# Kernel tuning notes

Measured on AMD Instinct MI355X. Metric: run time of the kernel, lower is better.

Reference implementation:

```python
import jax, jax.numpy as jnp
import numpy as np

N = 50000
E = 800000
DESC = 256
IN_CH = DESC + 64  # 320
HEADS = 4
HC = 64  # hidden_channels // heads
HID = HEADS * HC  # 256


def _lin(k, fan_in, fan_out):
    kw, kb = jax.random.split(k)
    s = 1.0 / np.sqrt(fan_in)
    W = jax.random.uniform(kw, (fan_in, fan_out), minval=-s, maxval=s, dtype=jnp.float32)
    b = jax.random.uniform(kb, (fan_out,), minval=-s, maxval=s, dtype=jnp.float32)
    return W, b


def setup_inputs() -> dict:
    key = jax.random.key(0)
    ks = jax.random.split(key, 16)
    x = jax.random.normal(ks[0], (N, DESC), dtype=jnp.float32)
    kpts = jax.random.uniform(ks[1], (N, 2), dtype=jnp.float32) * jnp.array([1216.0, 352.0])
    pts_3d = jax.random.uniform(ks[2], (N, 3), dtype=jnp.float32) * 10.0
    edge_index = jax.random.randint(ks[3], (2, E), 0, N, dtype=jnp.int64)

    W1, b1 = _lin(ks[4], 3, 32)
    W2, b2 = _lin(ks[5], 32, 64)
    Wres, bres = _lin(ks[6], IN_CH, HID)
    Wl, bl = _lin(ks[7], IN_CH, HID)
    Wr, br = _lin(ks[8], IN_CH, HID)
    We, _ = _lin(ks[9], 3, HID)
    att = jax.random.normal(ks[10], (HEADS, HC), dtype=jnp.float32) * 0.1
    conv_bias = jnp.zeros((HID,), dtype=jnp.float32)
    gamma = jnp.ones((HID,), dtype=jnp.float32)
    beta = jnp.zeros((HID,), dtype=jnp.float32)
    Wp, bp = _lin(ks[11], HID, 256)
    return dict(x=x, kpts=kpts, pts_3d=pts_3d, edge_index=edge_index,
                W1=W1, b1=b1, W2=W2, b2=b2, Wres=Wres, bres=bres,
                Wl=Wl, bl=bl, Wr=Wr, br=br, We=We, att=att, conv_bias=conv_bias,
                gamma=gamma, beta=beta, Wp=Wp, bp=bp)


def reference(x, kpts, pts_3d, edge_index, W1, b1, W2, b2, Wres, bres,
              Wl, bl, Wr, br, We, att, conv_bias, gamma, beta, Wp, bp):
    n = x.shape[0]
    norm_uv = kpts / jnp.array([1216.0, 352.0], dtype=kpts.dtype)
    depth = pts_3d[:, 2:3]
    pos_input = jnp.concatenate([norm_uv, depth], axis=-1)  # [N,3]
    pos_feat = jax.nn.silu(pos_input @ W1 + b1) @ W2 + b2   # [N,64]
    node_x = jnp.concatenate([x, pos_feat], axis=-1)        # [N,320]

    src, dst = edge_index[0], edge_index[1]
    rel_uv = norm_uv[dst] - norm_uv[src]                    # [E,2]
    dist = jnp.linalg.norm(rel_uv, axis=-1, keepdims=True)  # [E,1]
    edge_attr = jnp.concatenate([rel_uv, dist], axis=-1)    # [E,3]

    identity = node_x @ Wres + bres                         # [N,256]

    # GATv2Conv (share_weights=False, concat=True, neg_slope=0.2, no self-loops)
    x_l = (node_x @ Wl + bl).reshape(n, HEADS, HC)
    x_r = (node_x @ Wr + br).reshape(n, HEADS, HC)
    e_feat = (edge_attr @ We).reshape(-1, HEADS, HC)        # [E,H,C]

    m = x_l[src] + x_r[dst] + e_feat                        # [E,H,C]
    m = jnp.where(m >= 0, m, 0.2 * m)                       # LeakyReLU(0.2)
    logits = jnp.einsum('ehc,hc->eh', m, att)               # [E,H]

    # segment softmax over incoming edges of each dst node
    lmax = jax.ops.segment_max(logits, dst, num_segments=n)  # [N,H]
    ex = jnp.exp(logits - lmax[dst])
    denom = jax.ops.segment_sum(ex, dst, num_segments=n)     # [N,H]
    alpha = ex / (denom[dst] + 1e-16)                        # [E,H]

    msg = x_l[src] * alpha[:, :, None]                       # [E,H,C]
    out = jax.ops.segment_sum(msg, dst, num_segments=n).reshape(n, HID) + conv_bias

    # LayerNorm
    mu = out.mean(-1, keepdims=True)
    var = out.var(-1, keepdims=True)
    out = (out - mu) / jnp.sqrt(var + 1e-5) * gamma + beta

    out = jax.nn.silu(out)
    out = out + identity
    out = out @ Wp + bp
    return out, alpha
```

## Files before the change

### kernel.cpp

```cpp
#include <hip/hip_runtime.h>
#include <math.h>

#define NN 50000
#define NPAD 50048
#define EE 800000
#define HIDC 256
#define INCH 320

typedef __attribute__((ext_vector_type(8))) short bf16x8;
typedef __attribute__((ext_vector_type(4))) float f32x4;
typedef __attribute__((ext_vector_type(2))) float f32x2;

static __device__ __forceinline__ float4 ld4(const float* p){ return *(const float4*)p; }

static __device__ __forceinline__ unsigned short f2b(float f){
  union { float f; unsigned u; } v; v.f = f;
  unsigned r = v.u + 0x7fffu + ((v.u >> 16) & 1u);
  return (unsigned short)(r >> 16);
}
static __device__ __forceinline__ float b2f(unsigned short u){
  union { unsigned u; float f; } v; v.u = ((unsigned)u) << 16; return v.f;
}
static __device__ __forceinline__ float rlane_f(float v, int l){
  return __uint_as_float(__builtin_amdgcn_readlane(__float_as_uint(v), l));
}
static __device__ __forceinline__ int rlane_i(int v, int l){
  return __builtin_amdgcn_readlane(v, l);
}
static __device__ __forceinline__ f32x2 unpk(unsigned u){
  f32x2 r;
  r.x = __uint_as_float(u << 16);
  r.y = __uint_as_float(u & 0xffff0000u);
  return r;
}
static __device__ __forceinline__ f32x2 fma2(f32x2 a, f32x2 b, f32x2 c){
  return __builtin_elementwise_fma(a, b, c);
}
static __device__ __forceinline__ f32x2 max2(f32x2 a, f32x2 b){
  return __builtin_elementwise_max(a, b);
}
static __device__ __forceinline__ f32x2 set2(float v){ f32x2 r; r.x = v; r.y = v; return r; }

typedef const __attribute__((address_space(1))) unsigned int* gas_u32;
typedef __attribute__((address_space(3))) unsigned int* las_u32;
static __device__ __forceinline__ void gload_lds16(const void* g, void* l){
  __builtin_amdgcn_global_load_lds((gas_u32)g, (las_u32)l, 16, 0, 0);
}

__global__ void cvt_x_kernel(const float* __restrict__ x, unsigned short* __restrict__ nodex)
{
  int t = blockIdx.x*blockDim.x + threadIdx.x;
  int row = t >> 6;
  if (row >= NN) return;
  int c4 = (t & 63) * 4;
  float4 v = ld4(x + (size_t)row*256 + c4);
  ushort4 o;
  o.x = f2b(v.x); o.y = f2b(v.y); o.z = f2b(v.z); o.w = f2b(v.w);
  *(ushort4*)(nodex + (size_t)row*320 + c4) = o;
}

__global__ void node_mlp_kernel(const float* __restrict__ kpts,
                                const float* __restrict__ pts3d,
                                const float* __restrict__ W1, const float* __restrict__ b1,
                                const float* __restrict__ W2, const float* __restrict__ b2,
                                unsigned short* __restrict__ nodex)
{
  int i = blockIdx.x*blockDim.x + threadIdx.x;
  if (i >= NN) return;
  float u = kpts[2*i]   * (1.0f/1216.0f);
  float v = kpts[2*i+1] * (1.0f/352.0f);
  float d = pts3d[3*i+2];
  float h[32];
#pragma unroll
  for (int j=0;j<32;++j){
    float t = u*W1[j] + v*W1[32+j] + d*W1[64+j] + b1[j];
    h[j] = t / (1.0f + __expf(-t));
  }
  for (int o=0;o<64;o+=4){
    float s0=b2[o], s1=b2[o+1], s2=b2[o+2], s3=b2[o+3];
#pragma unroll
    for (int j=0;j<32;++j){
      float hj = h[j];
      const float* w = W2 + j*64 + o;
      s0 += hj*w[0]; s1 += hj*w[1]; s2 += hj*w[2]; s3 += hj*w[3];
    }
    ushort4 r; r.x=f2b(s0); r.y=f2b(s1); r.z=f2b(s2); r.w=f2b(s3);
    *(ushort4*)(nodex + (size_t)i*320 + 256 + o) = r;
  }
}

__global__ void cvt_w_kernel(const float* __restrict__ Wres, const float* __restrict__ Wl,
                             const float* __restrict__ Wr,   const float* __restrict__ Wp,
                             const float* __restrict__ bres, const float* __restrict__ bl,
                             const float* __restrict__ br,
                             unsigned short* __restrict__ wt, float* __restrict__ biascat)
{
  int t = blockIdx.x*blockDim.x + threadIdx.x;
  if (t < 245760) {
    int which = t / 81920;
    int rem = t % 81920;
    int n = rem / 320, k = rem % 320;
    const float* W = (which == 0) ? Wres : (which == 1) ? Wl : Wr;
    wt[(size_t)which*81920 + rem] = f2b(W[(size_t)k*256 + n]);
  } else if (t < 311296) {
    int r = t - 245760;
    int n = r / 256, k = r % 256;
    wt[245760 + r] = f2b(Wp[(size_t)k*256 + n]);
  } else {
    int r = t - 311296;
    const float* src = (r < 256) ? bres : (r < 512) ? bl : br;
    biascat[r] = src[r & 255];
  }
}

#define GK 32
__global__ __launch_bounds__(256) void mfma_gemm_kernel(
    const unsigned short* __restrict__ A,
    const unsigned short* __restrict__ BT,
    const float* __restrict__ bias,
    float* __restrict__ Cf,
    unsigned short* __restrict__ Cx1,
    unsigned short* __restrict__ Cx2,
    int M, int K)
{
  __shared__ unsigned short Als[128*GK];
  __shared__ unsigned short Bls[128*GK];
  int tid = threadIdx.x;
  int lane = tid & 63, wave = tid >> 6;
  int wm = (wave >> 1) * 64, wn = (wave & 1) * 64;
  int row0 = blockIdx.x * 128, col0 = blockIdx.y * 128;

  f32x4 acc[4][4];
#pragma unroll
  for (int i=0;i<4;++i)
#pragma unroll
    for (int j=0;j<4;++j){ acc[i][j].x=0.f; acc[i][j].y=0.f; acc[i][j].z=0.f; acc[i][j].w=0.f; }

  int fm = lane & 15;
  int fk = (lane >> 4) * 8;

  for (int k0 = 0; k0 < K; k0 += GK) {
#pragma unroll
    for (int it = 0; it < 2; ++it) {
      int seg = it*256 + tid;
      int r = seg >> 2, kb = (seg & 3) * 8;
      gload_lds16(A  + (size_t)(row0 + r)*K + k0 + kb, Als + (it*256 + wave*64)*8);
      gload_lds16(BT + (size_t)(col0 + r)*K + k0 + kb, Bls + (it*256 + wave*64)*8);
    }
    __syncthreads();

    bf16x8 af[4], bfr[4];
#pragma unroll
    for (int mi=0; mi<4; ++mi)
      af[mi] = *(const bf16x8*)&Als[(wm + mi*16 + fm)*GK + fk];
#pragma unroll
    for (int ni=0; ni<4; ++ni)
      bfr[ni] = *(const bf16x8*)&Bls[(wn + ni*16 + fm)*GK + fk];
#pragma unroll
    for (int mi=0; mi<4; ++mi)
#pragma unroll
      for (int ni=0; ni<4; ++ni)
        acc[mi][ni] = __builtin_amdgcn_mfma_f32_16x16x32_bf16(af[mi], bfr[ni], acc[mi][ni], 0, 0, 0);
    __syncthreads();
  }

  int seg = col0 >> 8;
  int colbase = col0 - seg*256;
  int cn = lane & 15, cr = (lane >> 4) * 4;
#pragma unroll
  for (int ni=0; ni<4; ++ni){
    int gcol = col0 + wn + ni*16 + cn;
    int col  = colbase + wn + ni*16 + cn;
    float bb = bias[gcol];
#pragma unroll
    for (int mi=0; mi<4; ++mi){
#pragma unroll
      for (int r=0; r<4; ++r){
        int row = row0 + wm + mi*16 + cr + r;
        if (row < M){
          float v = acc[mi][ni][r] + bb;
          if (seg == 0)      Cf [(size_t)row*256 + col] = v;
          else if (seg == 1) Cx1[(size_t)row*256 + col] = f2b(v);
          else               Cx2[(size_t)row*256 + col] = f2b(v);
        }
      }
    }
  }
}

__global__ void hist_kernel(const int* __restrict__ ei, int* __restrict__ deg){
  int e = blockIdx.x*blockDim.x + threadIdx.x;
  if (e < EE) atomicAdd(&deg[ei[EE + e]], 1);
}

__global__ __launch_bounds__(1024) void scan1_kernel(const int* __restrict__ deg,
                                                     int* __restrict__ incl, int* __restrict__ bsum){
  __shared__ int wsums[16];
  int t = threadIdx.x, lane = t & 63, w = t >> 6;
  int i = blockIdx.x*1024 + t;
  int v = (i < NN) ? deg[i] : 0;
  int sc = v;
#pragma unroll
  for (int off = 1; off < 64; off <<= 1) {
    int o = __shfl_up(sc, off, 64);
    if (lane >= off) sc += o;
  }
  if (lane == 63) wsums[w] = sc;
  __syncthreads();
  if (w == 0) {
    int ws = (lane < 16) ? wsums[lane] : 0;
#pragma unroll
    for (int off = 1; off < 16; off <<= 1) {
      int o = __shfl_up(ws, off, 64);
      if (lane >= off) ws += o;
    }
    if (lane < 16) wsums[lane] = ws;
  }
  __syncthreads();
  int woff = (w > 0) ? wsums[w-1] : 0;
  if (i < NN) incl[i] = sc + woff;
  if (t == 1023) bsum[blockIdx.x] = woff + sc;
}

__global__ void scan2_kernel(int* __restrict__ bsum, int nblk){
  int lane = threadIdx.x;
  int v = (lane < nblk) ? bsum[lane] : 0;
#pragma unroll
  for (int off = 1; off < 64; off <<= 1) {
    int o = __shfl_up(v, off, 64);
    if (lane >= off) v += o;
  }
  if (lane < nblk) bsum[lane] = v;
}

__global__ __launch_bounds__(1024) void scan3_kernel(const int* __restrict__ incl,
                                                     const int* __restrict__ deg,
                                                     const int* __restrict__ bsum,
                                                     int* __restrict__ rowptr, int* __restrict__ cursor,
                                                     int nblk){
  int i = blockIdx.x*1024 + threadIdx.x;
  if (i < NN) {
    int b = blockIdx.x;
    int prev = (b > 0) ? bsum[b-1] : 0;
    int ex = prev + incl[i] - deg[i];
    rowptr[i] = ex;
    cursor[i] = ex;
  }
  if (i == 0) rowptr[NN] = bsum[nblk-1];
}

__global__ void scatter_kernel(const int* __restrict__ ei, const float* __restrict__ kpts,
                               int* __restrict__ cursor,
                               float4* __restrict__ edata, int* __restrict__ eord){
  int e = blockIdx.x*blockDim.x + threadIdx.x;
  if (e >= EE) return;
  int s = ei[e];
  int d = ei[EE + e];
  int pos = atomicAdd(&cursor[d], 1);
  float su = kpts[2*s]   * (1.0f/1216.0f);
  float sv = kpts[2*s+1] * (1.0f/352.0f);
  float du = kpts[2*d]   * (1.0f/1216.0f);
  float dv = kpts[2*d+1] * (1.0f/352.0f);
  float ru = du - su, rv = dv - sv;
  float dist = sqrtf(ru*ru + rv*rv);
  float4 ed; ed.x = ru; ed.y = rv; ed.z = dist; ed.w = __int_as_float(s);
  edata[pos] = ed;
  eord[pos] = e;
}

#define LOAD8(Q, B0)                                               \
  if ((B0) < cnt) {                                                \
    _Pragma("unroll")                                              \
    for (int t = 0; t < 8; ++t) {                                  \
      int sj = rlane_i(s, ((B0) + t) & 63);                        \
      Q[t] = *(const uint2*)(xlp + ((size_t)sj << 8));             \
    }                                                              \
  }

#define PROC8(Q, B0)                                               \
  _Pragma("unroll")                                                \
  for (int t = 0; t < 8; ++t) {                                    \
    int j = (B0) + t;                                              \
    if (j < cnt) {                                                 \
      float ruj = rlane_f(ed.x, j);                                \
      float rvj = rlane_f(ed.y, j);                                \
      float dj  = rlane_f(ed.z, j);                                \
      f32x2 x01 = unpk(Q[t].x), x23 = unpk(Q[t].y);                \
      f32x2 t01 = fma2(set2(ruj), we0a, xr01);                     \
      t01 = fma2(set2(rvj), we1a, t01);                            \
      t01 = fma2(set2(dj),  we2a, t01);                            \
      t01 = t01 + x01;                                             \
      f32x2 t23 = fma2(set2(ruj), we0b, xr23);                     \
      t23 = fma2(set2(rvj), we1b, t23);                            \
      t23 = fma2(set2(dj),  we2b, t23);                            \
      t23 = t23 + x23;                                             \
      t01 = max2(t01, t01*0.2f);                                   \
      t23 = max2(t23, t23*0.2f);                                   \
      f32x2 pd = t01*atta;                                         \
      pd = fma2(t23, attb, pd);                                    \
      float p = pd.x + pd.y;                                       \
      p += __shfl_xor(p, 1, 64);                                   \
      p += __shfl_xor(p, 2, 64);                                   \
      p += __shfl_xor(p, 4, 64);                                   \
      p += __shfl_xor(p, 8, 64);                                   \
      float exv = __expf(p);                                       \
      denom += exv;                                                \
      int ej = rlane_i(e, j);                                      \
      if ((lane & 15) == 0) alpha_out[(size_t)ej*4 + head] = exv;  \
      f32x2 ex2 = set2(exv);                                       \
      agg01 = fma2(ex2, x01, agg01);                               \
      agg23 = fma2(ex2, x23, agg23);                               \
    }                                                              \
  }

__global__ __launch_bounds__(256) void node_attn_kernel(
    const float4* __restrict__ edata, const int* __restrict__ eord,
    const unsigned short* __restrict__ xl, const unsigned short* __restrict__ xr,
    const float* __restrict__ We, const float* __restrict__ att,
    const float* __restrict__ cbias, const float* __restrict__ gamma,
    const float* __restrict__ beta,
    const int* __restrict__ rowptr,
    const float* __restrict__ identity,
    float* __restrict__ alpha_out, float* __restrict__ denom_buf,
    unsigned short* __restrict__ hbuf)
{
  int wid  = threadIdx.x >> 6;
  int lane = threadIdx.x & 63;
  int v = blockIdx.x*4 + wid;
  if (v >= NN) return;
  int c0 = lane*4;
  int head = lane >> 4;

  f32x2 we0a, we0b, we1a, we1b, we2a, we2b, atta, attb;
  we0a.x = We[c0];       we0a.y = We[c0+1];       we0b.x = We[c0+2];       we0b.y = We[c0+3];
  we1a.x = We[256+c0];   we1a.y = We[256+c0+1];   we1b.x = We[256+c0+2];   we1b.y = We[256+c0+3];
  we2a.x = We[512+c0];   we2a.y = We[512+c0+1];   we2b.x = We[512+c0+2];   we2b.y = We[512+c0+3];
  atta.x = att[c0];      atta.y = att[c0+1];      attb.x = att[c0+2];      attb.y = att[c0+3];
  uint2 xrq = *(const uint2*)(xr + (size_t)v*256 + c0);
  f32x2 xr01 = unpk(xrq.x), xr23 = unpk(xrq.y);
  const unsigned short* xlp = xl + c0;

  int rs = rowptr[v], re = rowptr[v+1];
  int deg = re - rs;

  float denom = 0.f;
  f32x2 agg01 = set2(0.f), agg23 = set2(0.f);

  for (int base = 0; base < deg; base += 64) {
    int cnt = min(64, deg - base);
    float4 ed; ed.x = 0.f; ed.y = 0.f; ed.z = 0.f; ed.w = __int_as_float(0);
    int e = 0;
    if (lane < cnt) {
      ed = edata[rs + base + lane];
      e  = eord [rs + base + lane];
    }
    int s = __float_as_int(ed.w);

    uint2 qa[8], qb[8];
    LOAD8(qa, 0);
    for (int b0 = 0; b0 < cnt; b0 += 16) {
      LOAD8(qb, b0 + 8);
      PROC8(qa, b0);
      LOAD8(qa, b0 + 16);
      PROC8(qb, b0 + 8);
    }
  }

  float rdenom = 1.0f / (denom + 1e-16f);
  if ((lane & 15) == 0) denom_buf[(size_t)v*4 + head] = denom;

  float a0 = agg01.x*rdenom + cbias[c0];
  float a1 = agg01.y*rdenom + cbias[c0+1];
  float a2 = agg23.x*rdenom + cbias[c0+2];
  float a3 = agg23.y*rdenom + cbias[c0+3];

  float ps  = a0 + a1 + a2 + a3;
  float ps2 = a0*a0 + a1*a1 + a2*a2 + a3*a3;
#pragma unroll
  for (int off = 1; off < 64; off <<= 1) {
    ps  += __shfl_xor(ps,  off, 64);
    ps2 += __shfl_xor(ps2, off, 64);
  }
  float mu  = ps  * (1.0f/256.0f);
  float var = ps2 * (1.0f/256.0f) - mu*mu;
  float rstd = rsqrtf(var + 1e-5f);
  float4 g  = ld4(gamma + c0);
  float4 b  = ld4(beta  + c0);
  float4 idv = ld4(identity + (size_t)v*256 + c0);
  float y0 = (a0 - mu)*rstd*g.x + b.x;
  float y1 = (a1 - mu)*rstd*g.y + b.y;
  float y2 = (a2 - mu)*rstd*g.z + b.z;
  float y3 = (a3 - mu)*rstd*g.w + b.w;
  y0 = y0 / (1.0f + __expf(-y0)) + idv.x;
  y1 = y1 / (1.0f + __expf(-y1)) + idv.y;
  y2 = y2 / (1.0f + __expf(-y2)) + idv.z;
  y3 = y3 / (1.0f + __expf(-y3)) + idv.w;
  ushort4 hq; hq.x=f2b(y0); hq.y=f2b(y1); hq.z=f2b(y2); hq.w=f2b(y3);
  *(ushort4*)(hbuf + (size_t)v*256 + c0) = hq;
}

__global__ void alpha_fin_kernel(const int* __restrict__ ei, const float* __restrict__ denom_buf,
                                 float* __restrict__ alpha)
{
  int e = blockIdx.x*blockDim.x + threadIdx.x;
  if (e >= EE) return;
  int d = ei[EE + e];
  float4 dn = ld4(denom_buf + (size_t)d*4);
  float4 a = ld4(alpha + (size_t)e*4);
  a.x /= (dn.x + 1e-16f);
  a.y /= (dn.y + 1e-16f);
  a.z /= (dn.z + 1e-16f);
  a.w /= (dn.w + 1e-16f);
  *(float4*)(alpha + (size_t)e*4) = a;
}

extern "C" void kernel_launch(void* const* d_in, const int* in_sizes, int n_in,
                              void* d_out, int out_size, void* d_ws, size_t ws_size,
                              hipStream_t stream)
{
  const float* x      = (const float*)d_in[0];
  const float* kpts   = (const float*)d_in[1];
  const float* pts3d  = (const float*)d_in[2];
  const int*   ei     = (const int*)d_in[3];
  const float* W1     = (const float*)d_in[4];
  const float* b1     = (const float*)d_in[5];
  const float* W2     = (const float*)d_in[6];
  const float* b2     = (const float*)d_in[7];
  const float* Wres   = (const float*)d_in[8];
  const float* bres   = (const float*)d_in[9];
  const float* Wl     = (const float*)d_in[10];
  const float* bl     = (const float*)d_in[11];
  const float* Wr     = (const float*)d_in[12];
  const float* br     = (const float*)d_in[13];
  const float* We     = (const float*)d_in[14];
  const float* att    = (const float*)d_in[15];
  const float* cbias  = (const float*)d_in[16];
  const float* gamma  = (const float*)d_in[17];
  const float* beta   = (const float*)d_in[18];
  const float* Wp     = (const float*)d_in[19];
  const float* bp     = (const float*)d_in[20];

  float* out       = (float*)d_out;
  float* alpha_out = out + (size_t)NN*HIDC;

  float* wsf = (float*)d_ws;
  float*          identity = wsf;
  unsigned short* xl       = (unsigned short*)(wsf + 12800000);
  unsigned short* xr       = (unsigned short*)(wsf + 19206144);
  unsigned short* nodex    = (unsigned short*)(wsf + 25612288);
  unsigned short* hbuf     = (unsigned short*)(wsf + 25612288);
  unsigned short* wt       = (unsigned short*)(wsf + 33619968);
  float*          biascat  = wsf + 33775616;
  float*          denomb   = wsf + 33776384;
  float4*         edata    = (float4*)(wsf + 33976384);
  int*            eord     = (int*)(wsf + 37176384);
  int*            incl     = (int*)(wsf + 37176384);
  int*            deg      = (int*)(wsf + 37976384);
  int*            rowptr   = (int*)(wsf + 38026384);
  int*            cursor   = (int*)(wsf + 38076385);
  int*            bsum     = (int*)(wsf + 38126385);

  unsigned short* wtcat = wt;
  unsigned short* wtp   = wt + 245760;

  cvt_x_kernel<<<12500, 256, 0, stream>>>(x, nodex);
  node_mlp_kernel<<<(NN+255)/256, 256, 0, stream>>>(kpts, pts3d, W1, b1, W2, b2, nodex);
  cvt_w_kernel<<<1219, 256, 0, stream>>>(Wres, Wl, Wr, Wp, bres, bl, br, wt, biascat);

  dim3 g3(NPAD/128, 6);
  mfma_gemm_kernel<<<g3, 256, 0, stream>>>(nodex, wtcat, biascat, identity, xl, xr, NN, INCH);

  hipMemsetAsync(deg, 0, NN*sizeof(int), stream);
  hist_kernel<<<(EE+255)/256, 256, 0, stream>>>(ei, deg);
  int nblk = (NN + 1023) / 1024;
  scan1_kernel<<<nblk, 1024, 0, stream>>>(deg, incl, bsum);
  scan2_kernel<<<1, 64, 0, stream>>>(bsum, nblk);
  scan3_kernel<<<nblk, 1024, 0, stream>>>(incl, deg, bsum, rowptr, cursor, nblk);
  scatter_kernel<<<(EE+255)/256, 256, 0, stream>>>(ei, kpts, cursor, edata, eord);

  node_attn_kernel<<<(NN+3)/4, 256, 0, stream>>>(edata, eord, xl, xr, We, att,
                                                 cbias, gamma, beta,
                                                 rowptr, identity,
                                                 alpha_out, denomb, hbuf);
  alpha_fin_kernel<<<(EE+255)/256, 256, 0, stream>>>(ei, denomb, alpha_out);

  dim3 g1(NPAD/128, 2);
  mfma_gemm_kernel<<<g1, 256, 0, stream>>>(hbuf, wtp, bp, out, nullptr, nullptr, NN, HIDC);
}
```

Baseline: 552.1 us.

## Process two edges per wavefront using half-waves with wider per-lane loads

The node attention kernel now splits each 64-lane wavefront into two 32-lane halves. Each half processes a different incoming edge, and each lane covers 8 channels with 16-byte loads instead of 4 channels with 8-byte loads. Per-edge data is now loaded per lane with a software prefetch pipeline that runs two pairs ahead, replacing the batched readlane broadcasts. The goal is to halve the serial per-edge iteration count and the shuffle-reduction depth per edge. The cost is a cross-half reduction at the end, more registers, and idle lanes when the degree is odd.

```diff
diff --git a/kernel.cpp b/kernel.cpp
--- a/kernel.cpp
+++ b/kernel.cpp
@@ -20,12 +20,6 @@
 }
 static __device__ __forceinline__ float b2f(unsigned short u){
   union { unsigned u; float f; } v; v.u = ((unsigned)u) << 16; return v.f;
-}
-static __device__ __forceinline__ float rlane_f(float v, int l){
-  return __uint_as_float(__builtin_amdgcn_readlane(__float_as_uint(v), l));
-}
-static __device__ __forceinline__ int rlane_i(int v, int l){
-  return __builtin_amdgcn_readlane(v, l);
 }
 static __device__ __forceinline__ f32x2 unpk(unsigned u){
   f32x2 r;
@@ -268,49 +262,53 @@
   eord[pos] = e;
 }
 
-#define LOAD8(Q, B0)                                               \
-  if ((B0) < cnt) {                                                \
-    _Pragma("unroll")                                              \
-    for (int t = 0; t < 8; ++t) {                                  \
-      int sj = rlane_i(s, ((B0) + t) & 63);                        \
-      Q[t] = *(const uint2*)(xlp + ((size_t)sj << 8));             \
-    }                                                              \
-  }
-
-#define PROC8(Q, B0)                                               \
-  _Pragma("unroll")                                                \
-  for (int t = 0; t < 8; ++t) {                                    \
-    int j = (B0) + t;                                              \
-    if (j < cnt) {                                                 \
-      float ruj = rlane_f(ed.x, j);                                \
-      float rvj = rlane_f(ed.y, j);                                \
-      float dj  = rlane_f(ed.z, j);                                \
-      f32x2 x01 = unpk(Q[t].x), x23 = unpk(Q[t].y);                \
-      f32x2 t01 = fma2(set2(ruj), we0a, xr01);                     \
-      t01 = fma2(set2(rvj), we1a, t01);                            \
-      t01 = fma2(set2(dj),  we2a, t01);                            \
-      t01 = t01 + x01;                                             \
-      f32x2 t23 = fma2(set2(ruj), we0b, xr23);                     \
-      t23 = fma2(set2(rvj), we1b, t23);                            \
-      t23 = fma2(set2(dj),  we2b, t23);                            \
-      t23 = t23 + x23;                                             \
-      t01 = max2(t01, t01*0.2f);                                   \
-      t23 = max2(t23, t23*0.2f);                                   \
-      f32x2 pd = t01*atta;                                         \
-      pd = fma2(t23, attb, pd);                                    \
-      float p = pd.x + pd.y;                                       \
-      p += __shfl_xor(p, 1, 64);                                   \
-      p += __shfl_xor(p, 2, 64);                                   \
-      p += __shfl_xor(p, 4, 64);                                   \
-      p += __shfl_xor(p, 8, 64);                                   \
-      float exv = __expf(p);                                       \
-      denom += exv;                                                \
-      int ej = rlane_i(e, j);                                      \
-      if ((lane & 15) == 0) alpha_out[(size_t)ej*4 + head] = exv;  \
-      f32x2 ex2 = set2(exv);                                       \
-      agg01 = fma2(ex2, x01, agg01);                               \
-      agg23 = fma2(ex2, x23, agg23);                               \
-    }                                                              \
+
+#define LOAD_ED(P, ED, EV)                                           \
+  {                                                                  \
+    int j_ = 2*(P) + half;                                           \
+    int idx_ = rs + ((j_ < deg) ? j_ : 0);                           \
+    ED = edata[idx_];                                                \
+    EV = eord[idx_];                                                 \
+  }
+
+#define LOAD_Q(ED, Q)                                                \
+  {                                                                  \
+    int s_ = __float_as_int((ED).w);                                 \
+    Q = *(const uint4*)(xlp + ((size_t)s_ << 8));                    \
+  }
+
+#define PROC_E(P, ED, EV, Q)                                         \
+  {                                                                  \
+    bool act = (2*(P) + half) < deg;                                 \
+    f32x2 x0 = unpk((Q).x), x1 = unpk((Q).y);                        \
+    f32x2 x2 = unpk((Q).z), x3 = unpk((Q).w);                        \
+    f32x2 ru = set2((ED).x), rv = set2((ED).y), dd = set2((ED).z);   \
+    f32x2 t0 = fma2(ru, w0[0], xr4[0]);                              \
+    f32x2 t1 = fma2(ru, w0[1], xr4[1]);                              \
+    f32x2 t2 = fma2(ru, w0[2], xr4[2]);                              \
+    f32x2 t3 = fma2(ru, w0[3], xr4[3]);                              \
+    t0 = fma2(rv, w1[0], t0); t1 = fma2(rv, w1[1], t1);              \
+    t2 = fma2(rv, w1[2], t2); t3 = fma2(rv, w1[3], t3);              \
+    t0 = fma2(dd, w2[0], t0); t1 = fma2(dd, w2[1], t1);              \
+    t2 = fma2(dd, w2[2], t2); t3 = fma2(dd, w2[3], t3);              \
+    t0 = t0 + x0; t1 = t1 + x1; t2 = t2 + x2; t3 = t3 + x3;          \
+    t0 = max2(t0, t0*0.2f); t1 = max2(t1, t1*0.2f);                  \
+    t2 = max2(t2, t2*0.2f); t3 = max2(t3, t3*0.2f);                  \
+    f32x2 pd = t0*at4[0];                                            \
+    pd = fma2(t1, at4[1], pd);                                       \
+    pd = fma2(t2, at4[2], pd);                                       \
+    pd = fma2(t3, at4[3], pd);                                       \
+    float p = pd.x + pd.y;                                           \
+    p += __shfl_xor(p, 1, 64);                                       \
+    p += __shfl_xor(p, 2, 64);                                       \
+    p += __shfl_xor(p, 4, 64);                                       \
+    float exv = act ? __expf(p) : 0.0f;                              \
+    denom += exv;                                                    \
+    if (act && (li & 7) == 0)                                        \
+      alpha_out[(size_t)(EV)*4 + head] = exv;                        \
+    f32x2 ex2 = set2(exv);                                           \
+    agg[0] = fma2(ex2, x0, agg[0]); agg[1] = fma2(ex2, x1, agg[1]);  \
+    agg[2] = fma2(ex2, x2, agg[2]); agg[3] = fma2(ex2, x3, agg[3]);  \
   }
 
 __global__ __launch_bounds__(256) void node_attn_kernel(
@@ -328,75 +326,120 @@
   int lane = threadIdx.x & 63;
   int v = blockIdx.x*4 + wid;
   if (v >= NN) return;
-  int c0 = lane*4;
-  int head = lane >> 4;
-
-  f32x2 we0a, we0b, we1a, we1b, we2a, we2b, atta, attb;
-  we0a.x = We[c0];       we0a.y = We[c0+1];       we0b.x = We[c0+2];       we0b.y = We[c0+3];
-  we1a.x = We[256+c0];   we1a.y = We[256+c0+1];   we1b.x = We[256+c0+2];   we1b.y = We[256+c0+3];
-  we2a.x = We[512+c0];   we2a.y = We[512+c0+1];   we2b.x = We[512+c0+2];   we2b.y = We[512+c0+3];
-  atta.x = att[c0];      atta.y = att[c0+1];      attb.x = att[c0+2];      attb.y = att[c0+3];
-  uint2 xrq = *(const uint2*)(xr + (size_t)v*256 + c0);
-  f32x2 xr01 = unpk(xrq.x), xr23 = unpk(xrq.y);
+  int li   = lane & 31;
+  int half = lane >> 5;
+  int c0   = li * 8;
+  int head = li >> 3;
+
+  f32x2 w0[4], w1[4], w2[4], at4[4], xr4[4];
+  {
+    float4 a = ld4(We + c0),        b = ld4(We + c0 + 4);
+    w0[0].x=a.x; w0[0].y=a.y; w0[1].x=a.z; w0[1].y=a.w;
+    w0[2].x=b.x; w0[2].y=b.y; w0[3].x=b.z; w0[3].y=b.w;
+    a = ld4(We + 256 + c0); b = ld4(We + 256 + c0 + 4);
+    w1[0].x=a.x; w1[0].y=a.y; w1[1].x=a.z; w1[1].y=a.w;
+    w1[2].x=b.x; w1[2].y=b.y; w1[3].x=b.z; w1[3].y=b.w;
+    a = ld4(We + 512 + c0); b = ld4(We + 512 + c0 + 4);
+    w2[0].x=a.x; w2[0].y=a.y; w2[1].x=a.z; w2[1].y=a.w;
+    w2[2].x=b.x; w2[2].y=b.y; w2[3].x=b.z; w2[3].y=b.w;
+    a = ld4(att + c0);      b = ld4(att + c0 + 4);
+    at4[0].x=a.x; at4[0].y=a.y; at4[1].x=a.z; at4[1].y=a.w;
+    at4[2].x=b.x; at4[2].y=b.y; at4[3].x=b.z; at4[3].y=b.w;
+  }
+  {
+    uint4 xrq = *(const uint4*)(xr + (size_t)v*256 + c0);
+    xr4[0] = unpk(xrq.x); xr4[1] = unpk(xrq.y);
+    xr4[2] = unpk(xrq.z); xr4[3] = unpk(xrq.w);
+  }
   const unsigned short* xlp = xl + c0;
 
   int rs = rowptr[v], re = rowptr[v+1];
   int deg = re - rs;
+  int npairs = (deg + 1) >> 1;
 
   float denom = 0.f;
-  f32x2 agg01 = set2(0.f), agg23 = set2(0.f);
-
-  for (int base = 0; base < deg; base += 64) {
-    int cnt = min(64, deg - base);
-    float4 ed; ed.x = 0.f; ed.y = 0.f; ed.z = 0.f; ed.w = __int_as_float(0);
-    int e = 0;
-    if (lane < cnt) {
-      ed = edata[rs + base + lane];
-      e  = eord [rs + base + lane];
+  f32x2 agg[4];
+  agg[0]=set2(0.f); agg[1]=set2(0.f); agg[2]=set2(0.f); agg[3]=set2(0.f);
+
+  if (npairs > 0) {
+    float4 ed0, ed1, ed2;
+    int e0 = 0, e1 = 0, e2 = 0;
+    uint4 q0, q1;
+    ed1.x=0.f; ed1.y=0.f; ed1.z=0.f; ed1.w=0.f; ed2 = ed1;
+    q1.x=0u; q1.y=0u; q1.z=0u; q1.w=0u;
+
+    LOAD_ED(0, ed0, e0);
+    LOAD_Q(ed0, q0);
+    if (npairs > 1) { LOAD_ED(1, ed1, e1); }
+
+    for (int p = 0; p < npairs; ++p) {
+      if (p + 2 < npairs) { LOAD_ED(p+2, ed2, e2); }
+      if (p + 1 < npairs) { LOAD_Q(ed1, q1); }
+      PROC_E(p, ed0, e0, q0);
+      ed0 = ed1; e0 = e1; q0 = q1;
+      ed1 = ed2; e1 = e2;
     }
-    int s = __float_as_int(ed.w);
-
-    uint2 qa[8], qb[8];
-    LOAD8(qa, 0);
-    for (int b0 = 0; b0 < cnt; b0 += 16) {
-      LOAD8(qb, b0 + 8);
-      PROC8(qa, b0);
-      LOAD8(qa, b0 + 16);
-      PROC8(qb, b0 + 8);
-    }
-  }
-
+  }
+
+#pragma unroll
+  for (int k = 0; k < 4; ++k) {
+    agg[k].x += __shfl_xor(agg[k].x, 32, 64);
+    agg[k].y += __shfl_xor(agg[k].y, 32, 64);
+  }
+  denom += __shfl_xor(denom, 32, 64);
+  if (half == 0 && (li & 7) == 0) denom_buf[(size_t)v*4 + head] = denom;
   float rdenom = 1.0f / (denom + 1e-16f);
-  if ((lane & 15) == 0) denom_buf[(size_t)v*4 + head] = denom;
-
-  float a0 = agg01.x*rdenom + cbias[c0];
-  float a1 = agg01.y*rdenom + cbias[c0+1];
-  float a2 = agg23.x*rdenom + cbias[c0+2];
-  float a3 = agg23.y*rdenom + cbias[c0+3];
-
-  float ps  = a0 + a1 + a2 + a3;
-  float ps2 = a0*a0 + a1*a1 + a2*a2 + a3*a3;
-#pragma unroll
-  for (int off = 1; off < 64; off <<= 1) {
+
+  float4 cb0 = ld4(cbias + c0), cb1 = ld4(cbias + c0 + 4);
+  float a0 = agg[0].x*rdenom + cb0.x;
+  float a1 = agg[0].y*rdenom + cb0.y;
+  float a2 = agg[1].x*rdenom + cb0.z;
+  float a3 = agg[1].y*rdenom + cb0.w;
+  float a4 = agg[2].x*rdenom + cb1.x;
+  float a5 = agg[2].y*rdenom + cb1.y;
+  float a6 = agg[3].x*rdenom + cb1.z;
+  float a7 = agg[3].y*rdenom + cb1.w;
+
+  float ps  = ((a0+a1)+(a2+a3)) + ((a4+a5)+(a6+a7));
+  float ps2 = ((a0*a0+a1*a1)+(a2*a2+a3*a3)) + ((a4*a4+a5*a5)+(a6*a6+a7*a7));
+#pragma unroll
+  for (int off = 1; off < 32; off <<= 1) {
     ps  += __shfl_xor(ps,  off, 64);
     ps2 += __shfl_xor(ps2, off, 64);
   }
   float mu  = ps  * (1.0f/256.0f);
   float var = ps2 * (1.0f/256.0f) - mu*mu;
   float rstd = rsqrtf(var + 1e-5f);
-  float4 g  = ld4(gamma + c0);
-  float4 b  = ld4(beta  + c0);
-  float4 idv = ld4(identity + (size_t)v*256 + c0);
-  float y0 = (a0 - mu)*rstd*g.x + b.x;
-  float y1 = (a1 - mu)*rstd*g.y + b.y;
-  float y2 = (a2 - mu)*rstd*g.z + b.z;
-  float y3 = (a3 - mu)*rstd*g.w + b.w;
-  y0 = y0 / (1.0f + __expf(-y0)) + idv.x;
-  y1 = y1 / (1.0f + __expf(-y1)) + idv.y;
-  y2 = y2 / (1.0f + __expf(-y2)) + idv.z;
-  y3 = y3 / (1.0f + __expf(-y3)) + idv.w;
-  ushort4 hq; hq.x=f2b(y0); hq.y=f2b(y1); hq.z=f2b(y2); hq.w=f2b(y3);
-  *(ushort4*)(hbuf + (size_t)v*256 + c0) = hq;
+  float4 g0  = ld4(gamma + c0), g1 = ld4(gamma + c0 + 4);
+  float4 bb0 = ld4(beta  + c0), bb1 = ld4(beta  + c0 + 4);
+  float4 id0 = ld4(identity + (size_t)v*256 + c0);
+  float4 id1 = ld4(identity + (size_t)v*256 + c0 + 4);
+
+  float y0 = (a0 - mu)*rstd*g0.x + bb0.x;
+  float y1 = (a1 - mu)*rstd*g0.y + bb0.y;
+  float y2 = (a2 - mu)*rstd*g0.z + bb0.z;
+  float y3 = (a3 - mu)*rstd*g0.w + bb0.w;
+  float y4 = (a4 - mu)*rstd*g1.x + bb1.x;
+  float y5 = (a5 - mu)*rstd*g1.y + bb1.y;
+  float y6 = (a6 - mu)*rstd*g1.z + bb1.z;
+  float y7 = (a7 - mu)*rstd*g1.w + bb1.w;
+  y0 = y0 / (1.0f + __expf(-y0)) + id0.x;
+  y1 = y1 / (1.0f + __expf(-y1)) + id0.y;
+  y2 = y2 / (1.0f + __expf(-y2)) + id0.z;
+  y3 = y3 / (1.0f + __expf(-y3)) + id0.w;
+  y4 = y4 / (1.0f + __expf(-y4)) + id1.x;
+  y5 = y5 / (1.0f + __expf(-y5)) + id1.y;
+  y6 = y6 / (1.0f + __expf(-y6)) + id1.z;
+  y7 = y7 / (1.0f + __expf(-y7)) + id1.w;
+
+  if (half == 0) {
+    uint4 hq;
+    hq.x = (unsigned)f2b(y0) | ((unsigned)f2b(y1) << 16);
+    hq.y = (unsigned)f2b(y2) | ((unsigned)f2b(y3) << 16);
+    hq.z = (unsigned)f2b(y4) | ((unsigned)f2b(y5) << 16);
+    hq.w = (unsigned)f2b(y6) | ((unsigned)f2b(y7) << 16);
+    *(uint4*)(hbuf + (size_t)v*256 + c0) = hq;
+  }
 }
 
 __global__ void alpha_fin_kernel(const int* __restrict__ ei, const float* __restrict__ denom_buf,
```

Measured after the change: 564.3 us. 2.2% more time.
